# Performance work log

Hardware: AMD Instinct MI355X
Metric: run time of the kernel (lower is better)

Reference implementation:

```python
import jax, jax.numpy as jnp
import numpy as np

# Dims: B=32 batch, C=64 feat channels, Np=192 priors, No=72 row offsets,
# Ns=36 pooled sample points (maxpool kernel 2), Hd=64 fc hidden.
B, C, Np, No, Hd = 32, 64, 192, 72, 64
NS_POOL = 2  # n_offsets // sample_points
REG_DIM = No + 4  # reg_layers output


def bilinear_sample(feat, gx, gy):
    """torch F.grid_sample(align_corners=True) equivalent for in-range coords.
    feat: [B,C,H,W]; gx,gy: [B,Np,S] normalized to [-1,1]. -> [B,C,Np,S]."""
    Bb, Cc, H, W = feat.shape
    ix = (gx + 1.0) * 0.5 * (W - 1)
    iy = (gy + 1.0) * 0.5 * (H - 1)
    ix0f = jnp.floor(ix); iy0f = jnp.floor(iy)
    wx = ix - ix0f; wy = iy - iy0f
    ix0 = jnp.clip(ix0f.astype(jnp.int32), 0, W - 1)
    iy0 = jnp.clip(iy0f.astype(jnp.int32), 0, H - 1)
    ix1 = jnp.clip(ix0 + 1, 0, W - 1)
    iy1 = jnp.clip(iy0 + 1, 0, H - 1)
    ff = feat.reshape(Bb, Cc, H * W)
    S = gx.shape[1] * gx.shape[2]
    def gather(iy_, ix_):
        idx = (iy_ * W + ix_).reshape(Bb, 1, S)
        g = jnp.take_along_axis(ff, jnp.broadcast_to(idx, (Bb, Cc, S)), axis=2)
        return g.reshape(Bb, Cc, gx.shape[1], gx.shape[2])
    v00 = gather(iy0, ix0); v01 = gather(iy0, ix1)
    v10 = gather(iy1, ix0); v11 = gather(iy1, ix1)
    wx = wx[:, None]; wy = wy[:, None]  # broadcast over C
    return (v00 * (1 - wx) * (1 - wy) + v01 * wx * (1 - wy)
            + v10 * (1 - wx) * wy + v11 * wx * wy)


def _mlp2(h, Ws, bs):
    # two stacked Linear+ReLU layers (num_fc=2)
    for i in range(2):
        h = jax.nn.relu(h @ Ws[i] + bs[i])
    return h


def setup_inputs() -> dict:
    key = jax.random.key(0)
    ks = jax.random.split(key, 24)
    w = lambda k, sh: jax.random.normal(k, sh, dtype=jnp.float32) * 0.05
    return {
        "x0": jax.random.normal(ks[0], (B, C, 40, 100), dtype=jnp.float32),
        "x1": jax.random.normal(ks[1], (B, C, 20, 50), dtype=jnp.float32),
        "x2": jax.random.normal(ks[2], (B, C, 10, 25), dtype=jnp.float32),
        "prior_xs0": jax.random.uniform(ks[3], (Np, No), dtype=jnp.float32),
        "l_weight": w(ks[4], (No,)),              # self.l embedding, sigmoid gate
        "lsgi_w": w(ks[5], (3, C, C)),            # per-stage lsgi projection
        "fc_w": w(ks[6], (C, Hd)), "fc_b": w(ks[7], (Hd,)),
        "cls_w": w(ks[8], (2, Hd, Hd)), "cls_b": w(ks[9], (2, Hd)),
        "cls_ow": w(ks[10], (Hd, 2)), "cls_ob": w(ks[11], (2,)),
        "reg_w": w(ks[12], (2, Hd, Hd)), "reg_b": w(ks[13], (2, Hd)),
        "reg_ow": w(ks[14], (Hd, REG_DIM)), "reg_ob": w(ks[15], (REG_DIM,)),
        "loc_w": w(ks[16], (2, Hd, Hd)), "loc_b": w(ks[17], (2, Hd)),
        "loc_ow": w(ks[18], (Hd, 1)), "loc_ob": w(ks[19], (1,)),
    }


def reference(x0, x1, x2, prior_xs0, l_weight, lsgi_w, fc_w, fc_b,
              cls_w, cls_b, cls_ow, cls_ob, reg_w, reg_b, reg_ow, reg_ob,
              loc_w, loc_b, loc_ow, loc_ob):
    pyramid = [x2, x1, x0]  # reversed: coarsest level first (stage 0)
    prior_feat_ys = jnp.linspace(1.0, 0.0, No, dtype=jnp.float32)
    gy = jnp.broadcast_to((prior_feat_ys * 2.0 - 1.0)[None, None, :], (B, Np, No))
    prior_xs = jnp.broadcast_to(prior_xs0[None], (B, Np, No))
    gate = jax.nn.sigmoid(l_weight)[:, None]  # [No,1]
    stage_feats = []
    outs = []
    for s in range(3):
        gx = prior_xs * 2.0 - 1.0
        pooled = bilinear_sample(pyramid[s], gx, gy)          # [B,C,Np,No]
        pooled = jnp.transpose(pooled, (0, 2, 3, 1)) * gate   # [B,Np,No,C]
        pooled = jax.nn.relu(jnp.einsum('bnoc,cd->bnod', pooled, lsgi_w[s]))
        # MaxPool2d kernel (2,1) over the offset axis -> Ns=36 sample points
        comp = pooled.reshape(B, Np, No // NS_POOL, NS_POOL, C).max(axis=3)
        stage_feats.append(comp)
        # cross-stage fusion (global head): mean over stages and sample points
        fused = jnp.stack(stage_feats, 0).mean(axis=0).mean(axis=2)  # [B,Np,C]
        fc = jax.nn.relu(fused @ fc_w + fc_b)                        # [B,Np,Hd]
        cls = _mlp2(fc, cls_w, cls_b) @ cls_ow + cls_ob              # [B,Np,2]
        reg = _mlp2(fc, reg_w, reg_b) @ reg_ow + reg_ob              # [B,Np,No+4]
        loc = _mlp2(fc, loc_w, loc_b) @ loc_ow + loc_ob              # [B,Np,1]
        outs.append(jnp.concatenate([cls, reg, loc], axis=-1))      # [B,Np,79]
        # refine anchors for next stage from predicted xs
        prior_xs = jax.nn.sigmoid(reg[..., 4:])
    return jnp.stack(outs, axis=0)  # [3,B,Np,79]
```

## Files before the change

### kernel.cpp

```cpp
#include <hip/hip_runtime.h>
#include <hip/hip_bf16.h>

#define Bq   32
#define Cq   64
#define NPq  192
#define NOq  72
#define PTS  (NPq * NOq)
#define NTB  (PTS / 16)
#define FRAG_PER_B ((size_t)NTB * 2 * 64 * 8)
#define REGD 76
#define OUTD 79
#define HSTR 68

typedef __attribute__((ext_vector_type(8))) short short8;
typedef __attribute__((ext_vector_type(4))) float float4v;

__device__ inline unsigned short f2bf(float x) {
    __hip_bfloat16 h = __float2bfloat16(x);
    return *reinterpret_cast<unsigned short*>(&h);
}

template<int H, int W>
__global__ __launch_bounds__(256) void rowblend_kernel(
    const float* __restrict__ feat,
    const float* __restrict__ xsrc,
    const int xstride,
    const float* __restrict__ lw,
    unsigned short* __restrict__ pooled,
    const int b0)
{
    constexpr int Wp  = W + 1;
    constexpr int OCH = 8;
    __shared__ float sT[8 * OCH * Wp];
    __shared__ float sWy[NOq], sGate[NOq];
    __shared__ int   sIy0W[NOq], sIy1W[NOq];

    const int tid = threadIdx.x;
    const int bl  = blockIdx.x / 72;
    const int rem = blockIdx.x - bl * 72;
    const int cg  = rem & 7;
    const int oc  = rem >> 3;
    const int b   = b0 + bl;
    const int c0  = cg * 8;

    if (tid < NOq) {
        const float ys = 1.0f - (float)tid * (1.0f / 71.0f);
        const float iy = ys * (float)(H - 1);
        const float fy = floorf(iy);
        sWy[tid] = iy - fy;
        int iy0 = (int)fy; iy0 = iy0 < 0 ? 0 : (iy0 > H - 1 ? H - 1 : iy0);
        const int iy1 = (iy0 + 1 > H - 1) ? H - 1 : iy0 + 1;
        sIy0W[tid] = iy0 * W;
        sIy1W[tid] = iy1 * W;
        sGate[tid] = 1.0f / (1.0f + __expf(-lw[tid]));
    }
    __syncthreads();

    const float* fbase = feat + (size_t)(b * Cq + c0) * (H * W);
    const float* xp    = xsrc + (size_t)xstride * b;
    unsigned short* pb = pooled + (size_t)bl * FRAG_PER_B;
    const int ks   = cg >> 2;
    const int lofs = 16 * (cg & 3);

    constexpr int TOT = 8 * OCH * W;
    for (int idx = tid; idx < TOT; idx += 256) {
        const int row = idx / W;
        const int x   = idx - row * W;
        const int c   = row >> 3;
        const int ol  = row & 7;
        const int o   = oc * OCH + ol;
        const float wy = sWy[o];
        const float* f = fbase + c * (H * W);
        const float v = (1.0f - wy) * f[sIy0W[o] + x] + wy * f[sIy1W[o] + x];
        sT[row * Wp + x] = v * sGate[o];
    }
    __syncthreads();
    if (tid < 8 * OCH) sT[tid * Wp + W] = sT[tid * Wp + W - 1];
    __syncthreads();

    #pragma unroll
    for (int i = 0; i < 6; ++i) {
        const int ptl = i * 256 + tid;
        const int n   = ptl >> 3;
        const int ol  = ptl & 7;
        const int o   = oc * OCH + ol;
        const int pt  = n * NOq + o;
        float ixf = xp[pt] * (float)(W - 1);
        ixf = fminf(fmaxf(ixf, 0.0f), (float)(W - 1));
        const float fx = floorf(ixf);
        const float wx = ixf - fx;
        const int ix0 = (int)fx;
        union { unsigned short u[8]; short8 v; } pk;
        #pragma unroll
        for (int c = 0; c < 8; ++c) {
            const float a0 = sT[(c * OCH + ol) * Wp + ix0];
            const float a1 = sT[(c * OCH + ol) * Wp + ix0 + 1];
            pk.u[c] = f2bf(a0 + wx * (a1 - a0));
        }
        const int nt = pt >> 4;
        const int l  = (pt & 15) + lofs;
        *(short8*)(pb + ((((size_t)nt * 2 + ks) * 64 + l) << 3)) = pk.v;
    }
}

__global__ __launch_bounds__(256) void mfma_pool_kernel(
    const unsigned short* __restrict__ pooled,
    const float* __restrict__ lsgi,
    float* __restrict__ sumFeat,
    const int b0, const int accumulate)
{
    const int tid  = threadIdx.x;
    const int w    = tid >> 6;
    const int lane = tid & 63;
    const int bl    = blockIdx.x / 24;
    const int ng    = blockIdx.x - bl * 24;
    const int npair = ng * 4 + w;
    const int b     = b0 + bl;

    short8 wf[4][2];
    {
        const int kb = ((lane >> 4) & 3) * 8;
        const int dl = lane & 15;
        #pragma unroll
        for (int ks = 0; ks < 2; ++ks)
            #pragma unroll
            for (int dt = 0; dt < 4; ++dt) {
                union { unsigned short u[8]; short8 v; } pk;
                #pragma unroll
                for (int j = 0; j < 8; ++j)
                    pk.u[j] = f2bf(lsgi[(ks * 32 + kb + j) * 64 + dt * 16 + dl]);
                wf[dt][ks] = pk.v;
            }
    }

    const unsigned short* pbase = pooled + (size_t)bl * FRAG_PER_B;
    const int nt0 = npair * 9;

    float sums0[4] = {0.f, 0.f, 0.f, 0.f};
    float sums1[4] = {0.f, 0.f, 0.f, 0.f};

    #pragma unroll
    for (int ntl = 0; ntl < 9; ++ntl) {
        const size_t fbase = (((size_t)(nt0 + ntl) * 2) * 64 + lane) << 3;
        const short8 a0 = *(const short8*)(pbase + fbase);
        const short8 a1 = *(const short8*)(pbase + fbase + 512);
        const bool hi = (ntl * 16 + ((lane >> 4) * 4)) >= NOq;
        #pragma unroll
        for (int dt = 0; dt < 4; ++dt) {
            float4v c = {0.f, 0.f, 0.f, 0.f};
            c = __builtin_amdgcn_mfma_f32_16x16x32_bf16(a0, wf[dt][0], c, 0, 0, 0);
            c = __builtin_amdgcn_mfma_f32_16x16x32_bf16(a1, wf[dt][1], c, 0, 0, 0);
            const float pm0 = fmaxf(fmaxf(c[0], c[1]), 0.f);
            const float pm1 = fmaxf(fmaxf(c[2], c[3]), 0.f);
            const float add = pm0 + pm1;
            if (hi) sums1[dt] += add; else sums0[dt] += add;
        }
    }

    #pragma unroll
    for (int dt = 0; dt < 4; ++dt) {
        float v0 = sums0[dt], v1 = sums1[dt];
        v0 += __shfl_xor(v0, 16); v0 += __shfl_xor(v0, 32);
        v1 += __shfl_xor(v1, 16); v1 += __shfl_xor(v1, 32);
        sums0[dt] = v0; sums1[dt] = v1;
    }

    if (lane < 16) {
        const size_t row0 = (size_t)(b * NPq + npair * 2) * 64;
        #pragma unroll
        for (int dt = 0; dt < 4; ++dt) {
            const int d = dt * 16 + lane;
            float t0 = sums0[dt] * (1.0f / 36.0f);
            float t1 = sums1[dt] * (1.0f / 36.0f);
            float* p0 = sumFeat + row0 + d;
            float* p1 = sumFeat + row0 + 64 + d;
            if (accumulate) { t0 += *p0; t1 += *p1; }
            *p0 = t0; *p1 = t1;
        }
    }
}

__global__ __launch_bounds__(256) void head_kernel(
    const float* __restrict__ sumFeat, const float invS,
    const float* __restrict__ fc_w,  const float* __restrict__ fc_b,
    const float* __restrict__ cls_w, const float* __restrict__ cls_b,
    const float* __restrict__ cls_ow, const float* __restrict__ cls_ob,
    const float* __restrict__ reg_w, const float* __restrict__ reg_b,
    const float* __restrict__ reg_ow, const float* __restrict__ reg_ob,
    const float* __restrict__ loc_w, const float* __restrict__ loc_b,
    const float* __restrict__ loc_ow, const float* __restrict__ loc_ob,
    float* __restrict__ out, float* __restrict__ xs_next)
{
    __shared__ __align__(16) float sAct0[32 * HSTR];
    __shared__ __align__(16) float sAct1[32 * HSTR];
    __shared__ __align__(16) float sW0[4096];
    __shared__ __align__(16) float sW1[4864];

    const int tid = threadIdx.x;
    const int hb  = blockIdx.x % 3;
    const int pg  = blockIdx.x / 3;
    const int p0  = pg * 32;
    const int tm  = tid >> 4;
    const int tn  = tid & 15;

    const float* h_w  = (hb == 0) ? cls_w  : (hb == 1) ? reg_w  : loc_w;
    const float* h_b  = (hb == 0) ? cls_b  : (hb == 1) ? reg_b  : loc_b;
    const float* h_ow = (hb == 0) ? cls_ow : (hb == 1) ? reg_ow : loc_ow;
    const float* h_ob = (hb == 0) ? cls_ob : (hb == 1) ? reg_ob : loc_ob;
    const int ow_n    = (hb == 0) ? 128    : (hb == 1) ? 64 * REGD : 64;

    #pragma unroll
    for (int i = 0; i < 4; ++i)
        *(float4*)&sW0[(i * 256 + tid) * 4] = *(const float4*)&fc_w[(i * 256 + tid) * 4];
    for (int idx = tid; idx < 32 * 64; idx += 256) {
        const int p = idx >> 6, c = idx & 63;
        sAct0[p * HSTR + c] = sumFeat[(size_t)(p0 + p) * 64 + c] * invS;
    }

    auto do_gemm = [&](const float* src, float* dst, const float* wbuf,
                       const float* gb, const float* nextw, int nextn,
                       float* nextbuf) {
        __syncthreads();
        float4 pf[5];
        const int n4 = nextn >> 2;
        #pragma unroll
        for (int i = 0; i < 5; ++i) {
            const int idx = i * 256 + tid;
            if (idx < n4) pf[i] = *(const float4*)&nextw[idx * 4];
        }
        const float4 b4 = *(const float4*)&gb[4 * tn];
        float4 acc0 = b4, acc1 = b4;
        const float* r0 = src + (2 * tm) * HSTR;
        const float* r1 = r0 + HSTR;
        #pragma unroll 4
        for (int k4 = 0; k4 < 16; ++k4) {
            const float4 a0 = *(const float4*)&r0[4 * k4];
            const float4 a1 = *(const float4*)&r1[4 * k4];
            const float4 w0 = *(const float4*)&wbuf[(4 * k4 + 0) * 64 + 4 * tn];
            const float4 w1 = *(const float4*)&wbuf[(4 * k4 + 1) * 64 + 4 * tn];
            const float4 w2 = *(const float4*)&wbuf[(4 * k4 + 2) * 64 + 4 * tn];
            const float4 w3 = *(const float4*)&wbuf[(4 * k4 + 3) * 64 + 4 * tn];
            acc0.x += a0.x*w0.x + a0.y*w1.x + a0.z*w2.x + a0.w*w3.x;
            acc0.y += a0.x*w0.y + a0.y*w1.y + a0.z*w2.y + a0.w*w3.y;
            acc0.z += a0.x*w0.z + a0.y*w1.z + a0.z*w2.z + a0.w*w3.z;
            acc0.w += a0.x*w0.w + a0.y*w1.w + a0.z*w2.w + a0.w*w3.w;
            acc1.x += a1.x*w0.x + a1.y*w1.x + a1.z*w2.x + a1.w*w3.x;
            acc1.y += a1.x*w0.y + a1.y*w1.y + a1.z*w2.y + a1.w*w3.y;
            acc1.z += a1.x*w0.z + a1.y*w1.z + a1.z*w2.z + a1.w*w3.z;
            acc1.w += a1.x*w0.w + a1.y*w1.w + a1.z*w2.w + a1.w*w3.w;
        }
        float4 v0, v1;
        v0.x = fmaxf(acc0.x, 0.f); v0.y = fmaxf(acc0.y, 0.f);
        v0.z = fmaxf(acc0.z, 0.f); v0.w = fmaxf(acc0.w, 0.f);
        v1.x = fmaxf(acc1.x, 0.f); v1.y = fmaxf(acc1.y, 0.f);
        v1.z = fmaxf(acc1.z, 0.f); v1.w = fmaxf(acc1.w, 0.f);
        *(float4*)&dst[(2 * tm) * HSTR + 4 * tn]     = v0;
        *(float4*)&dst[(2 * tm + 1) * HSTR + 4 * tn] = v1;
        #pragma unroll
        for (int i = 0; i < 5; ++i) {
            const int idx = i * 256 + tid;
            if (idx < n4) *(float4*)&nextbuf[idx * 4] = pf[i];
        }
    };

    do_gemm(sAct0, sAct1, sW0, fc_b,      h_w,        4096, sW1);
    do_gemm(sAct1, sAct0, sW1, h_b,       h_w + 4096, 4096, sW0);
    do_gemm(sAct0, sAct1, sW0, h_b + 64,  h_ow,       ow_n, sW1);
    __syncthreads();

    if (hb == 0) {
        if (tid < 64) {
            const int p = tid >> 1, d = tid & 1;
            const float* row = &sAct1[p * HSTR];
            float z = h_ob[d];
            #pragma unroll 4
            for (int k4 = 0; k4 < 16; ++k4) {
                const float4 a = *(const float4*)&row[4 * k4];
                z += a.x * sW1[(4 * k4 + 0) * 2 + d] + a.y * sW1[(4 * k4 + 1) * 2 + d]
                   + a.z * sW1[(4 * k4 + 2) * 2 + d] + a.w * sW1[(4 * k4 + 3) * 2 + d];
            }
            out[(size_t)(p0 + p) * OUTD + d] = z;
        }
    } else if (hb == 1) {
        const int p  = tid & 31;
        const int jg = tid >> 5;
        const float* row = &sAct1[p * HSTR];
        float* orow = out + (size_t)(p0 + p) * OUTD;
        float* xsp  = xs_next + (size_t)(p0 + p) * NOq;
        for (int j = jg; j < REGD; j += 8) {
            float z = h_ob[j];
            #pragma unroll 4
            for (int k4 = 0; k4 < 16; ++k4) {
                const float4 a = *(const float4*)&row[4 * k4];
                z += a.x * sW1[(4 * k4 + 0) * REGD + j] + a.y * sW1[(4 * k4 + 1) * REGD + j]
                   + a.z * sW1[(4 * k4 + 2) * REGD + j] + a.w * sW1[(4 * k4 + 3) * REGD + j];
            }
            orow[2 + j] = z;
            if (j >= 4) xsp[j - 4] = 1.0f / (1.0f + __expf(-z));
        }
    } else {
        if (tid < 32) {
            const float* row = &sAct1[tid * HSTR];
            float z = h_ob[0];
            #pragma unroll 4
            for (int k4 = 0; k4 < 16; ++k4) {
                const float4 a = *(const float4*)&row[4 * k4];
                z += a.x * sW1[4 * k4] + a.y * sW1[4 * k4 + 1]
                   + a.z * sW1[4 * k4 + 2] + a.w * sW1[4 * k4 + 3];
            }
            out[(size_t)(p0 + tid) * OUTD + 78] = z;
        }
    }
}

extern "C" void kernel_launch(void* const* d_in, const int* in_sizes, int n_in,
                              void* d_out, int out_size, void* d_ws, size_t ws_size,
                              hipStream_t stream)
{
    const float* x0        = (const float*)d_in[0];
    const float* x1        = (const float*)d_in[1];
    const float* x2        = (const float*)d_in[2];
    const float* prior_xs0 = (const float*)d_in[3];
    const float* l_weight  = (const float*)d_in[4];
    const float* lsgi_w    = (const float*)d_in[5];
    const float* fc_w      = (const float*)d_in[6];
    const float* fc_b      = (const float*)d_in[7];
    const float* cls_w     = (const float*)d_in[8];
    const float* cls_b     = (const float*)d_in[9];
    const float* cls_ow    = (const float*)d_in[10];
    const float* cls_ob    = (const float*)d_in[11];
    const float* reg_w     = (const float*)d_in[12];
    const float* reg_b     = (const float*)d_in[13];
    const float* reg_ow    = (const float*)d_in[14];
    const float* reg_ob    = (const float*)d_in[15];
    const float* loc_w     = (const float*)d_in[16];
    const float* loc_b     = (const float*)d_in[17];
    const float* loc_ow    = (const float*)d_in[18];
    const float* loc_ob    = (const float*)d_in[19];

    float* out     = (float*)d_out;
    float* sumFeat = (float*)d_ws;
    float* xs      = sumFeat + (size_t)Bq * NPq * Cq;
    unsigned short* pooled = (unsigned short*)(xs + (size_t)Bq * PTS);

    const size_t fixed_bytes = ((size_t)Bq * NPq * Cq + (size_t)Bq * PTS) * 4;
    const size_t per_b       = FRAG_PER_B * 2;
    int Bc = Bq;
    if (ws_size < fixed_bytes + (size_t)Bq * per_b) {
        Bc = (int)((ws_size - fixed_bytes) / per_b);
        if (Bc < 1) Bc = 1;
        if (Bc > Bq) Bc = Bq;
    }

    for (int s = 0; s < 3; ++s) {
        const float* xsrc = (s == 0) ? prior_xs0 : xs;
        const int xstr    = (s == 0) ? 0 : PTS;
        for (int c0 = 0; c0 < Bq; c0 += Bc) {
            const int bc = (Bc < Bq - c0) ? Bc : (Bq - c0);
            if (s == 0)
                hipLaunchKernelGGL((rowblend_kernel<10, 25>), dim3(bc * 72), dim3(256), 0, stream,
                                   x2, xsrc, xstr, l_weight, pooled, c0);
            else if (s == 1)
                hipLaunchKernelGGL((rowblend_kernel<20, 50>), dim3(bc * 72), dim3(256), 0, stream,
                                   x1, xsrc, xstr, l_weight, pooled, c0);
            else
                hipLaunchKernelGGL((rowblend_kernel<40, 100>), dim3(bc * 72), dim3(256), 0, stream,
                                   x0, xsrc, xstr, l_weight, pooled, c0);
            hipLaunchKernelGGL(mfma_pool_kernel, dim3(bc * 24), dim3(256), 0, stream,
                               pooled, lsgi_w + s * 4096, sumFeat, c0, (s > 0) ? 1 : 0);
        }
        hipLaunchKernelGGL(head_kernel, dim3((Bq * NPq / 32) * 3), dim3(256), 0, stream,
                           sumFeat, 1.0f / (float)(s + 1),
                           fc_w, fc_b, cls_w, cls_b, cls_ow, cls_ob,
                           reg_w, reg_b, reg_ow, reg_ob,
                           loc_w, loc_b, loc_ow, loc_ob,
                           out + (size_t)s * Bq * NPq * OUTD, xs);
    }
}
```

Measured before the change: 282.7 us.

## Precompute row-blended bf16 tables once and fuse x-interpolation into MFMA pool

Replaces the per-stage rowblend kernel, which wrote a full bf16 fragment buffer for every point, with one up-front kernel. That kernel builds, for each batch, row offset and pyramid level, a gated, y-interpolated bf16 row table laid out channel-contiguous. The MFMA pool kernel now gathers the two neighbouring columns from the table, does the x-blend in registers and feeds MFMA directly, removing the large intermediate write and read and cutting launches. The trade-offs are an extra bf16 rounding before the x-blend, scattered gathers into the tables, and a table workspace whose size is no longer checked against ws_size.

```diff
diff --git a/kernel.cpp b/kernel.cpp
--- a/kernel.cpp
+++ b/kernel.cpp
@@ -6,8 +6,6 @@
 #define NPq  192
 #define NOq  72
 #define PTS  (NPq * NOq)
-#define NTB  (PTS / 16)
-#define FRAG_PER_B ((size_t)NTB * 2 * 64 * 8)
 #define REGD 76
 #define OUTD 79
 #define HSTR 68
@@ -19,103 +17,79 @@
     __hip_bfloat16 h = __float2bfloat16(x);
     return *reinterpret_cast<unsigned short*>(&h);
 }
-
-template<int H, int W>
-__global__ __launch_bounds__(256) void rowblend_kernel(
-    const float* __restrict__ feat,
-    const float* __restrict__ xsrc,
-    const int xstride,
+__device__ inline float bf2f(unsigned short u) {
+    unsigned int x = ((unsigned int)u) << 16;
+    float f;
+    __builtin_memcpy(&f, &x, 4);
+    return f;
+}
+
+__global__ __launch_bounds__(256) void build_tables_kernel(
+    const float* __restrict__ f0,
+    const float* __restrict__ f1,
+    const float* __restrict__ f2,
     const float* __restrict__ lw,
-    unsigned short* __restrict__ pooled,
-    const int b0)
+    unsigned short* __restrict__ t0,
+    unsigned short* __restrict__ t1,
+    unsigned short* __restrict__ t2)
 {
-    constexpr int Wp  = W + 1;
-    constexpr int OCH = 8;
-    __shared__ float sT[8 * OCH * Wp];
-    __shared__ float sWy[NOq], sGate[NOq];
-    __shared__ int   sIy0W[NOq], sIy1W[NOq];
+    __shared__ float sRow[64 * 101];
 
     const int tid = threadIdx.x;
-    const int bl  = blockIdx.x / 72;
-    const int rem = blockIdx.x - bl * 72;
-    const int cg  = rem & 7;
-    const int oc  = rem >> 3;
-    const int b   = b0 + bl;
-    const int c0  = cg * 8;
-
-    if (tid < NOq) {
-        const float ys = 1.0f - (float)tid * (1.0f / 71.0f);
-        const float iy = ys * (float)(H - 1);
-        const float fy = floorf(iy);
-        sWy[tid] = iy - fy;
-        int iy0 = (int)fy; iy0 = iy0 < 0 ? 0 : (iy0 > H - 1 ? H - 1 : iy0);
-        const int iy1 = (iy0 + 1 > H - 1) ? H - 1 : iy0 + 1;
-        sIy0W[tid] = iy0 * W;
-        sIy1W[tid] = iy1 * W;
-        sGate[tid] = 1.0f / (1.0f + __expf(-lw[tid]));
+    int bid = blockIdx.x;
+    const float* feat; unsigned short* tab; int H, W;
+    if (bid < 2304)      { feat = f0; tab = t0; H = 10; W = 25; }
+    else if (bid < 4608) { feat = f1; tab = t1; H = 20; W = 50;  bid -= 2304; }
+    else                 { feat = f2; tab = t2; H = 40; W = 100; bid -= 4608; }
+    const int b = bid / NOq;
+    const int o = bid - b * NOq;
+    const int Wp = W + 1;
+
+    const float ys = 1.0f - (float)o * (1.0f / 71.0f);
+    const float iy = ys * (float)(H - 1);
+    const float fy = floorf(iy);
+    const float wy = iy - fy;
+    int iy0 = (int)fy; iy0 = iy0 < 0 ? 0 : (iy0 > H - 1 ? H - 1 : iy0);
+    const int iy1 = (iy0 + 1 > H - 1) ? H - 1 : iy0 + 1;
+    const float gate = 1.0f / (1.0f + __expf(-lw[o]));
+
+    const float* fb = feat + (size_t)b * 64 * H * W;
+    const int iy0W = iy0 * W, iy1W = iy1 * W;
+
+    const int tot = 64 * W;
+    for (int idx = tid; idx < tot; idx += 256) {
+        const int c = idx / W;
+        const int x = idx - c * W;
+        const float* f = fb + c * (H * W);
+        sRow[c * Wp + x] = ((1.0f - wy) * f[iy0W + x] + wy * f[iy1W + x]) * gate;
     }
     __syncthreads();
 
-    const float* fbase = feat + (size_t)(b * Cq + c0) * (H * W);
-    const float* xp    = xsrc + (size_t)xstride * b;
-    unsigned short* pb = pooled + (size_t)bl * FRAG_PER_B;
-    const int ks   = cg >> 2;
-    const int lofs = 16 * (cg & 3);
-
-    constexpr int TOT = 8 * OCH * W;
-    for (int idx = tid; idx < TOT; idx += 256) {
-        const int row = idx / W;
-        const int x   = idx - row * W;
-        const int c   = row >> 3;
-        const int ol  = row & 7;
-        const int o   = oc * OCH + ol;
-        const float wy = sWy[o];
-        const float* f = fbase + c * (H * W);
-        const float v = (1.0f - wy) * f[sIy0W[o] + x] + wy * f[sIy1W[o] + x];
-        sT[row * Wp + x] = v * sGate[o];
-    }
-    __syncthreads();
-    if (tid < 8 * OCH) sT[tid * Wp + W] = sT[tid * Wp + W - 1];
-    __syncthreads();
-
-    #pragma unroll
-    for (int i = 0; i < 6; ++i) {
-        const int ptl = i * 256 + tid;
-        const int n   = ptl >> 3;
-        const int ol  = ptl & 7;
-        const int o   = oc * OCH + ol;
-        const int pt  = n * NOq + o;
-        float ixf = xp[pt] * (float)(W - 1);
-        ixf = fminf(fmaxf(ixf, 0.0f), (float)(W - 1));
-        const float fx = floorf(ixf);
-        const float wx = ixf - fx;
-        const int ix0 = (int)fx;
-        union { unsigned short u[8]; short8 v; } pk;
-        #pragma unroll
-        for (int c = 0; c < 8; ++c) {
-            const float a0 = sT[(c * OCH + ol) * Wp + ix0];
-            const float a1 = sT[(c * OCH + ol) * Wp + ix0 + 1];
-            pk.u[c] = f2bf(a0 + wx * (a1 - a0));
-        }
-        const int nt = pt >> 4;
-        const int l  = (pt & 15) + lofs;
-        *(short8*)(pb + ((((size_t)nt * 2 + ks) * 64 + l) << 3)) = pk.v;
-    }
-}
-
-__global__ __launch_bounds__(256) void mfma_pool_kernel(
-    const unsigned short* __restrict__ pooled,
+    unsigned short* to = tab + (size_t)(b * NOq + o) * Wp * 64;
+    const int tot2 = Wp * 64;
+    for (int idx = tid; idx < tot2; idx += 256) {
+        const int x = idx >> 6;
+        const int c = idx & 63;
+        const int xx = (x < W) ? x : (W - 1);
+        to[idx] = f2bf(sRow[c * Wp + xx]);
+    }
+}
+
+template<int W>
+__global__ __launch_bounds__(256) void fused_pool_kernel(
+    const unsigned short* __restrict__ tab,
+    const float* __restrict__ xsrc, const int xstride,
     const float* __restrict__ lsgi,
     float* __restrict__ sumFeat,
-    const int b0, const int accumulate)
+    const int accumulate)
 {
+    constexpr int Wp = W + 1;
     const int tid  = threadIdx.x;
     const int w    = tid >> 6;
     const int lane = tid & 63;
-    const int bl    = blockIdx.x / 24;
-    const int ng    = blockIdx.x - bl * 24;
+    const int b    = blockIdx.x / 24;
+    const int ng   = blockIdx.x - b * 24;
     const int npair = ng * 4 + w;
-    const int b     = b0 + bl;
 
     short8 wf[4][2];
     {
@@ -133,7 +107,10 @@
             }
     }
 
-    const unsigned short* pbase = pooled + (size_t)bl * FRAG_PER_B;
+    const unsigned short* tb = tab + (size_t)b * NOq * Wp * 64;
+    const float* xp = xsrc + (size_t)xstride * b;
+    const int m  = lane & 15;
+    const int kg = lane >> 4;
     const int nt0 = npair * 9;
 
     float sums0[4] = {0.f, 0.f, 0.f, 0.f};
@@ -141,15 +118,34 @@
 
     #pragma unroll
     for (int ntl = 0; ntl < 9; ++ntl) {
-        const size_t fbase = (((size_t)(nt0 + ntl) * 2) * 64 + lane) << 3;
-        const short8 a0 = *(const short8*)(pbase + fbase);
-        const short8 a1 = *(const short8*)(pbase + fbase + 512);
-        const bool hi = (ntl * 16 + ((lane >> 4) * 4)) >= NOq;
+        const int pt = (nt0 + ntl) * 16 + m;
+        const int o  = pt % NOq;
+        float ixf = xp[pt] * (float)(W - 1);
+        ixf = fminf(fmaxf(ixf, 0.0f), (float)(W - 1));
+        const float fx = floorf(ixf);
+        const float wx = ixf - fx;
+        const int ix0 = (int)fx;
+
+        const unsigned short* col = tb + ((size_t)o * Wp + ix0) * 64 + kg * 8;
+        union { unsigned short u[8]; short8 v; } t00, t01, t10, t11, a0, a1;
+        t00.v = *(const short8*)(col);
+        t01.v = *(const short8*)(col + 64);
+        t10.v = *(const short8*)(col + 32);
+        t11.v = *(const short8*)(col + 96);
+        #pragma unroll
+        for (int j = 0; j < 8; ++j) {
+            const float l0 = bf2f(t00.u[j]), h0 = bf2f(t01.u[j]);
+            const float l1 = bf2f(t10.u[j]), h1 = bf2f(t11.u[j]);
+            a0.u[j] = f2bf(l0 + wx * (h0 - l0));
+            a1.u[j] = f2bf(l1 + wx * (h1 - l1));
+        }
+
+        const bool hi = (ntl * 16 + (kg * 4)) >= NOq;
         #pragma unroll
         for (int dt = 0; dt < 4; ++dt) {
             float4v c = {0.f, 0.f, 0.f, 0.f};
-            c = __builtin_amdgcn_mfma_f32_16x16x32_bf16(a0, wf[dt][0], c, 0, 0, 0);
-            c = __builtin_amdgcn_mfma_f32_16x16x32_bf16(a1, wf[dt][1], c, 0, 0, 0);
+            c = __builtin_amdgcn_mfma_f32_16x16x32_bf16(a0.v, wf[dt][0], c, 0, 0, 0);
+            c = __builtin_amdgcn_mfma_f32_16x16x32_bf16(a1.v, wf[dt][1], c, 0, 0, 0);
             const float pm0 = fmaxf(fmaxf(c[0], c[1]), 0.f);
             const float pm1 = fmaxf(fmaxf(c[2], c[3]), 0.f);
             const float add = pm0 + pm1;
@@ -341,34 +337,26 @@
     float* out     = (float*)d_out;
     float* sumFeat = (float*)d_ws;
     float* xs      = sumFeat + (size_t)Bq * NPq * Cq;
-    unsigned short* pooled = (unsigned short*)(xs + (size_t)Bq * PTS);
-
-    const size_t fixed_bytes = ((size_t)Bq * NPq * Cq + (size_t)Bq * PTS) * 4;
-    const size_t per_b       = FRAG_PER_B * 2;
-    int Bc = Bq;
-    if (ws_size < fixed_bytes + (size_t)Bq * per_b) {
-        Bc = (int)((ws_size - fixed_bytes) / per_b);
-        if (Bc < 1) Bc = 1;
-        if (Bc > Bq) Bc = Bq;
-    }
+    unsigned short* tab0 = (unsigned short*)(xs + (size_t)Bq * PTS);
+    unsigned short* tab1 = tab0 + (size_t)Bq * NOq * 26  * 64;
+    unsigned short* tab2 = tab1 + (size_t)Bq * NOq * 51  * 64;
+
+    hipLaunchKernelGGL(build_tables_kernel, dim3(3 * Bq * NOq), dim3(256), 0, stream,
+                       x2, x1, x0, l_weight, tab0, tab1, tab2);
 
     for (int s = 0; s < 3; ++s) {
         const float* xsrc = (s == 0) ? prior_xs0 : xs;
         const int xstr    = (s == 0) ? 0 : PTS;
-        for (int c0 = 0; c0 < Bq; c0 += Bc) {
-            const int bc = (Bc < Bq - c0) ? Bc : (Bq - c0);
-            if (s == 0)
-                hipLaunchKernelGGL((rowblend_kernel<10, 25>), dim3(bc * 72), dim3(256), 0, stream,
-                                   x2, xsrc, xstr, l_weight, pooled, c0);
-            else if (s == 1)
-                hipLaunchKernelGGL((rowblend_kernel<20, 50>), dim3(bc * 72), dim3(256), 0, stream,
-                                   x1, xsrc, xstr, l_weight, pooled, c0);
-            else
-                hipLaunchKernelGGL((rowblend_kernel<40, 100>), dim3(bc * 72), dim3(256), 0, stream,
-                                   x0, xsrc, xstr, l_weight, pooled, c0);
-            hipLaunchKernelGGL(mfma_pool_kernel, dim3(bc * 24), dim3(256), 0, stream,
-                               pooled, lsgi_w + s * 4096, sumFeat, c0, (s > 0) ? 1 : 0);
-        }
+        if (s == 0)
+            hipLaunchKernelGGL((fused_pool_kernel<25>), dim3(Bq * 24), dim3(256), 0, stream,
+                               tab0, xsrc, xstr, lsgi_w + s * 4096, sumFeat, 0);
+        else if (s == 1)
+            hipLaunchKernelGGL((fused_pool_kernel<50>), dim3(Bq * 24), dim3(256), 0, stream,
+                               tab1, xsrc, xstr, lsgi_w + s * 4096, sumFeat, 1);
+        else
+            hipLaunchKernelGGL((fused_pool_kernel<100>), dim3(Bq * 24), dim3(256), 0, stream,
+                               tab2, xsrc, xstr, lsgi_w + s * 4096, sumFeat, 1);
+
         hipLaunchKernelGGL(head_kernel, dim3((Bq * NPq / 32) * 3), dim3(256), 0, stream,
                            sumFeat, 1.0f / (float)(s + 1),
                            fc_w, fc_b, cls_w, cls_b, cls_ow, cls_ob,
```

Result: no change. 284.6 us (+0.7%).
